# Performance work log

Measured on AMD Instinct MI355X. Metric: run time of the kernel, lower is better.

The kernel has to match this reference:

```python
import jax, jax.numpy as jnp
import numpy as np

B, S, D, H = 2, 2048, 1024, 16
HD = D // H  # head depth


def setup_inputs() -> dict:
    key = jax.random.key(0)
    ks = jax.random.split(key, 8)
    scale = 0.02
    K = jax.random.normal(ks[0], (B, S, D), jnp.float32)
    V = jax.random.normal(ks[1], (B, S, D), jnp.float32)
    Q = jax.random.normal(ks[2], (B, S, D), jnp.float32)
    # causal additive mask: 1.0 where attention is disallowed (strict upper triangle)
    mask = jnp.broadcast_to(
        jnp.triu(jnp.ones((S, S), jnp.float32), k=1)[None, None, :, :], (B, 1, S, S)
    )
    Wk = jax.random.normal(ks[3], (D, D), jnp.float32) * scale
    Wv = jax.random.normal(ks[4], (D, D), jnp.float32) * scale
    Wq = jax.random.normal(ks[5], (D, D), jnp.float32) * scale
    Wo = jax.random.normal(ks[6], (D, D), jnp.float32) * scale
    z = jnp.zeros((D,), jnp.float32)
    return {"K": K, "V": V, "Q": Q, "mask": mask,
            "Wk": Wk, "bk": z, "Wv": Wv, "bv": z,
            "Wq": Wq, "bq": z, "Wo": Wo, "bo": z}


def _split_heads(x):  # [B,S,D] -> [B,H,S,HD]
    return x.reshape(B, S, H, HD).transpose(0, 2, 1, 3)


def reference(K, V, Q, mask, Wk, bk, Wv, bv, Wq, bq, Wo, bo):
    k = _split_heads(K @ Wk + bk)
    v = _split_heads(V @ Wv + bv)
    q = _split_heads(Q @ Wq + bq)
    # NOTE: source scales by sqrt(d_model), not sqrt(head_depth)
    logits = jnp.einsum("bhqd,bhkd->bhqk", q, k) / jnp.sqrt(jnp.float32(D))
    logits = logits + mask * (-1e9)
    attn = jax.nn.softmax(logits, axis=-1)
    out = jnp.einsum("bhqk,bhkd->bhqd", attn, v)  # [B,H,S,HD]
    out = out.transpose(0, 2, 1, 3).reshape(B, S, D)
    return out @ Wo + bo
```

## Files before the change

kernel.cpp:

```cpp
#include <hip/hip_runtime.h>
#include <hip/hip_bf16.h>

typedef unsigned short u16;
typedef unsigned int u32;
typedef unsigned long long u64;
typedef __attribute__((ext_vector_type(8))) __bf16 bf16x8;
typedef __attribute__((ext_vector_type(4))) float f32x4;

#define SEQ 2048
#define DM 1024
#define NH 16
#define HDim 64

__device__ __forceinline__ float bf_lo(u32 u) { return __uint_as_float(u << 16); }
__device__ __forceinline__ float bf_hi(u32 u) { return __uint_as_float(u & 0xffff0000u); }
__device__ __forceinline__ u16 f2bf(float f) {
    u32 u = __float_as_uint(f);
    u32 r = (u + 0x7fffu + ((u >> 16) & 1u)) >> 16;
    return (u16)r;
}
__device__ __forceinline__ float bf2f(u16 h) { return __uint_as_float(((u32)h) << 16); }

__device__ __forceinline__ float fexp2(float x) {
#if __has_builtin(__builtin_amdgcn_exp2f)
    return __builtin_amdgcn_exp2f(x);
#else
    return __expf(x * 0.69314718056f);
#endif
}

#define GLD16(g, l)                                                         \
    __builtin_amdgcn_global_load_lds(                                       \
        (const __attribute__((address_space(1))) void*)(g),                 \
        (__attribute__((address_space(3))) void*)(l), 16, 0, 0)

#define VWAIT_BAR(N)                                                        \
    asm volatile("s_waitcnt vmcnt(" #N ")\n\ts_barrier" ::: "memory")
#define BAR_ONLY()  asm volatile("s_barrier" ::: "memory")

__device__ __forceinline__ bool detect_f32(const u32* q)
{
    const u32 w = q[threadIdx.x & 63];
    const int e0 = ((w & 0xffffu) >> 7) & 0xff;
    const int e1 = (w >> 23) & 0xff;
    const unsigned long long b = __ballot(e0 >= 0x90 || e1 >= 0x90);
    return b != 0ull;
}

__global__ __launch_bounds__(256)
void prep_all(const void* __restrict__ Qin, const void* __restrict__ Kin,
              const void* __restrict__ Vin,
              const void* __restrict__ w0, const void* __restrict__ w1,
              const void* __restrict__ w2, const void* __restrict__ w3,
              const void* __restrict__ b0, const void* __restrict__ b1,
              const void* __restrict__ b2, const void* __restrict__ b3,
              u16* __restrict__ Xall, u16* __restrict__ Wtall,
              u16* __restrict__ ball)
{
    __shared__ u16 T[64 * 66];
    const bool f = detect_f32((const u32*)Qin);
    const int t = threadIdx.x;
    const int bid = blockIdx.x;

    if (bid < 6144) {
        const int z = bid >> 11;
        const int bx = bid & 2047;
        const void* src = (z == 0) ? Qin : (z == 1) ? Kin : Vin;
        const size_t i0 = ((size_t)bx * 256 + t) * 8;
        u16* d = Xall + (size_t)z * 4194304 + i0;
        if (f) {
            const uint4* s = reinterpret_cast<const uint4*>((const float*)src + i0);
            uint4 a = s[0], b = s[1];
            u16 o[8];
            o[0] = f2bf(__uint_as_float(a.x)); o[1] = f2bf(__uint_as_float(a.y));
            o[2] = f2bf(__uint_as_float(a.z)); o[3] = f2bf(__uint_as_float(a.w));
            o[4] = f2bf(__uint_as_float(b.x)); o[5] = f2bf(__uint_as_float(b.y));
            o[6] = f2bf(__uint_as_float(b.z)); o[7] = f2bf(__uint_as_float(b.w));
            *reinterpret_cast<uint4*>(d) = *reinterpret_cast<const uint4*>(o);
        } else {
            *reinterpret_cast<uint4*>(d) =
                *reinterpret_cast<const uint4*>((const u16*)src + i0);
        }
    } else if (bid < 7168) {
        const int r = bid - 6144;
        const int z = r >> 8;
        const void* src = (z == 0) ? w0 : (z == 1) ? w1 : (z == 2) ? w2 : w3;
        const int n0 = ((r >> 4) & 15) * 64;
        const int k0 = (r & 15) * 64;
        const int c = t & 63, g = t >> 6;
        if (f) {
            const float* W = (const float*)src;
#pragma unroll
            for (int i = 0; i < 16; i++) {
                const int kl = g * 16 + i;
                T[kl * 66 + c] = f2bf(W[(size_t)(k0 + kl) * DM + n0 + c]);
            }
        } else {
            const u16* W = (const u16*)src;
#pragma unroll
            for (int i = 0; i < 16; i++) {
                const int kl = g * 16 + i;
                T[kl * 66 + c] = W[(size_t)(k0 + kl) * DM + n0 + c];
            }
        }
        __syncthreads();
        u16* dst = Wtall + (size_t)z * 1048576;
#pragma unroll
        for (int i = 0; i < 16; i++) {
            const int nl = g * 16 + i;
            dst[(size_t)(n0 + nl) * DM + k0 + c] = T[c * 66 + nl];
        }
    } else {
#pragma unroll
        for (int j = 0; j < 16; j++) {
            const int idx = t * 16 + j;
            const int z = idx >> 10, e = idx & 1023;
            const void* src = (z == 0) ? b0 : (z == 1) ? b1 : (z == 2) ? b2 : b3;
            ball[idx] = f ? f2bf(((const float*)src)[e]) : ((const u16*)src)[e];
        }
    }
}

__global__ __launch_bounds__(256)
void gemm128(const u16* __restrict__ Xall, const u16* __restrict__ Wtall,
             const u16* __restrict__ ball, u16* __restrict__ Yall)
{
    __shared__ __align__(16) u16 As[2][128 * 32];
    __shared__ __align__(16) u16 Bs[2][128 * 32];

    const int zz = blockIdx.z;
    const bool swp = (zz != 2);
    const u16* X  = Xall + (size_t)zz * 4194304;
    const u16* Wt = Wtall + (size_t)zz * 1048576;

    const int t    = threadIdx.x;
    const int w    = t >> 6;
    const int lane = t & 63;
    const int quad = lane >> 4;
    const int ln   = lane & 15;
    const int m0   = blockIdx.x * 128;
    const int n0   = blockIdx.y * 128;

    f32x4 acc[4][4];
#pragma unroll
    for (int i = 0; i < 4; i++)
#pragma unroll
        for (int j = 0; j < 4; j++) acc[i][j] = (f32x4){0.f, 0.f, 0.f, 0.f};

    const int swz = (lane >> 3) & 3;
    const u16* ag = X  + (size_t)(m0 + w * 32 + (lane >> 2)) * DM + ((lane & 3) ^ swz) * 8;
    const u16* bg = Wt + (size_t)(n0 + w * 32 + (lane >> 2)) * DM + ((lane & 3) ^ swz) * 8;

    const int wr = (w >> 1) * 64;
    const int wc = (w & 1) * 64;
    const int rs = (quad ^ ((ln >> 1) & 3)) * 8;

#define GSTAGE(B)                                        \
    {                                                    \
        GLD16(ag,           &As[B][w * 1024]);           \
        GLD16(ag + 16 * DM, &As[B][w * 1024 + 512]);     \
        GLD16(bg,           &Bs[B][w * 1024]);           \
        GLD16(bg + 16 * DM, &Bs[B][w * 1024 + 512]);     \
        ag += 32; bg += 32;                              \
    }

#define GCOMP(B)                                                              \
    {                                                                         \
        bf16x8 af[4], bfr[4];                                                 \
        _Pragma("unroll") for (int rt = 0; rt < 4; rt++)                      \
            af[rt] = *reinterpret_cast<const bf16x8*>(                        \
                &As[B][(wr + rt * 16 + ln) * 32 + rs]);                       \
        _Pragma("unroll") for (int ct = 0; ct < 4; ct++)                      \
            bfr[ct] = *reinterpret_cast<const bf16x8*>(                       \
                &Bs[B][(wc + ct * 16 + ln) * 32 + rs]);                       \
        if (swp) {                                                            \
            _Pragma("unroll") for (int rt = 0; rt < 4; rt++)                  \
                _Pragma("unroll") for (int ct = 0; ct < 4; ct++)              \
                    acc[rt][ct] = __builtin_amdgcn_mfma_f32_16x16x32_bf16(    \
                        bfr[ct], af[rt], acc[rt][ct], 0, 0, 0);               \
        } else {                                                              \
            _Pragma("unroll") for (int rt = 0; rt < 4; rt++)                  \
                _Pragma("unroll") for (int ct = 0; ct < 4; ct++)              \
                    acc[rt][ct] = __builtin_amdgcn_mfma_f32_16x16x32_bf16(    \
                        af[rt], bfr[ct], acc[rt][ct], 0, 0, 0);               \
        }                                                                     \
    }

    GSTAGE(0);
#pragma unroll 1
    for (int it = 0; it < 15; ++it) {
        GSTAGE(1);
        VWAIT_BAR(4);
        GCOMP(0);
        BAR_ONLY();
        GSTAGE(0);
        VWAIT_BAR(4);
        GCOMP(1);
        BAR_ONLY();
    }
    GSTAGE(1);
    VWAIT_BAR(4);
    GCOMP(0);
    BAR_ONLY();
    asm volatile("s_waitcnt vmcnt(0)" ::: "memory");
    __builtin_amdgcn_s_barrier();
    GCOMP(1);
#undef GSTAGE
#undef GCOMP

    u16* Y = Yall + (size_t)zz * 4194304;

    if (swp) {
        const float scale = (zz == 0) ? 0.04508422f : 1.0f;
#pragma unroll
        for (int ct = 0; ct < 4; ct++) {
            const int nb = n0 + wc + ct * 16 + quad * 4;
            const int h = nb >> 6, hd = nb & (HDim - 1);
            float bv[4];
#pragma unroll
            for (int r = 0; r < 4; r++) bv[r] = bf2f(ball[zz * 1024 + nb + r]);
#pragma unroll
            for (int rt = 0; rt < 4; rt++) {
                const int m = m0 + wr + rt * 16 + ln;
                const int b = m >> 11, s = m & (SEQ - 1);
                u16 o4[4];
#pragma unroll
                for (int r = 0; r < 4; r++)
                    o4[r] = f2bf((acc[rt][ct][r] + bv[r]) * scale);
                *reinterpret_cast<u64*>(
                    Y + (((size_t)(b * NH + h)) * SEQ + s) * HDim + hd) =
                    *reinterpret_cast<const u64*>(o4);
            }
        }
    } else {
#pragma unroll
        for (int ct = 0; ct < 4; ct++) {
            const int n = n0 + wc + ct * 16 + ln;
            const float bv = bf2f(ball[zz * 1024 + n]);
            const int h = n >> 6, hd = n & (HDim - 1);
#pragma unroll
            for (int rt = 0; rt < 4; rt++) {
                const int m = m0 + wr + rt * 16 + quad * 4;
                const int b = m >> 11, s = m & (SEQ - 1);
                u16 o4[4];
#pragma unroll
                for (int r = 0; r < 4; r++) o4[r] = f2bf(acc[rt][ct][r] + bv);
                *reinterpret_cast<u64*>(
                    Y + (((size_t)(b * NH + h) * HDim + hd) * SEQ + s)) =
                    *reinterpret_cast<const u64*>(o4);
            }
        }
    }
}

__device__ __forceinline__ void attn_tile2(
    const u16* __restrict__ Ks, const u16* __restrict__ Vs,
    u16* __restrict__ Ps, const bf16x8& qf0, const bf16x8& qf1,
    int kt, int qrow, int w, int quad, int ln, f32x4* o, float& l,
    bool diag)
{
    f32x4 s[4];
    __builtin_amdgcn_s_setprio(1);
#pragma unroll
    for (int ct = 0; ct < 4; ct++) {
        const u16* kr = &Ks[(ct * 16 + ln) * 72 + quad * 8];
        bf16x8 kf0 = *reinterpret_cast<const bf16x8*>(kr);
        bf16x8 kf1 = *reinterpret_cast<const bf16x8*>(kr + 32);
        f32x4 z = (f32x4){0.f, 0.f, 0.f, 0.f};
        z = __builtin_amdgcn_mfma_f32_16x16x32_bf16(kf0, qf0, z, 0, 0, 0);
        s[ct] = __builtin_amdgcn_mfma_f32_16x16x32_bf16(kf1, qf1, z, 0, 0, 0);
    }
    __builtin_amdgcn_s_setprio(0);
    const int kb = kt * 64 + quad * 4;
    float lacc = 0.f;
#pragma unroll
    for (int ct = 0; ct < 4; ct++) {
        float e0 = fexp2(s[ct][0]);
        float e1 = fexp2(s[ct][1]);
        float e2 = fexp2(s[ct][2]);
        float e3 = fexp2(s[ct][3]);
        if (diag) {
            const int kc = kb + ct * 16;
            e0 = (kc + 0 <= qrow) ? e0 : 0.f;
            e1 = (kc + 1 <= qrow) ? e1 : 0.f;
            e2 = (kc + 2 <= qrow) ? e2 : 0.f;
            e3 = (kc + 3 <= qrow) ? e3 : 0.f;
        }
        lacc += (e0 + e1) + (e2 + e3);
        u32 pk[2];
        asm("v_cvt_pk_bf16_f32 %0, %1, %2" : "=v"(pk[0]) : "v"(e0), "v"(e1));
        asm("v_cvt_pk_bf16_f32 %0, %1, %2" : "=v"(pk[1]) : "v"(e2), "v"(e3));
        *reinterpret_cast<u64*>(&Ps[(w * 16 + ln) * 72 + ct * 16 + quad * 4]) =
            *reinterpret_cast<const u64*>(pk);
    }
    l += lacc;
    __builtin_amdgcn_s_setprio(1);
#pragma unroll
    for (int ks = 0; ks < 2; ks++) {
        bf16x8 pf = *reinterpret_cast<const bf16x8*>(
            &Ps[(w * 16 + ln) * 72 + ks * 32 + quad * 8]);
#pragma unroll
        for (int nt = 0; nt < 4; nt++) {
            bf16x8 vf = *reinterpret_cast<const bf16x8*>(
                &Vs[(nt * 16 + ln) * 72 + ks * 32 + quad * 8]);
            o[nt] = __builtin_amdgcn_mfma_f32_16x16x32_bf16(pf, vf, o[nt], 0, 0, 0);
        }
    }
    __builtin_amdgcn_s_setprio(0);
}

__global__ __launch_bounds__(256)
void attn_split(const u16* __restrict__ qh, const u16* __restrict__ kh,
                const u16* __restrict__ vt, u16* __restrict__ Opart,
                float* __restrict__ Lpart)
{
    __shared__ __align__(16) u16 Ks[64 * 72];
    __shared__ __align__(16) u16 Vs[64 * 72];
    __shared__ __align__(16) u16 Ps[64 * 72];

    const int t    = threadIdx.x;
    const int L    = blockIdx.x + 16 * (blockIdx.y + 32 * blockIdx.z);
    const int xcd  = L & 7;
    const int slot = L >> 3;
    const int bh   = xcd + 8 * (slot >> 5);
    const int rr   = slot & 31;
    const int i    = rr & 15;
    const int c    = rr >> 4;

    const int w    = t >> 6;
    const int lane = t & 63;
    const int quad = lane >> 4;
    const int ln   = lane & 15;
    const int qtH  = 31 - i;
    const int qtL  = i;
    const int m    = (i >= 8) ? 8 : 16 - i;
    const int kt0  = c ? m : 0;
    const int kt1  = c ? (qtH + 1) : m;

    const size_t kbase = (size_t)bh * SEQ * HDim;
    const size_t vbase = (size_t)bh * HDim * SEQ;

    const u16* qrH = qh + kbase + (size_t)(qtH * 64 + w * 16 + ln) * HDim;
    const bf16x8 qfH0 = *reinterpret_cast<const bf16x8*>(qrH + quad * 8);
    const bf16x8 qfH1 = *reinterpret_cast<const bf16x8*>(qrH + 32 + quad * 8);
    const u16* qrL = qh + kbase + (size_t)(qtL * 64 + w * 16 + ln) * HDim;
    const bf16x8 qfL0 = *reinterpret_cast<const bf16x8*>(qrL + quad * 8);
    const bf16x8 qfL1 = *reinterpret_cast<const bf16x8*>(qrL + 32 + quad * 8);

    f32x4 oH[4], oL[4];
    float lH = 0.f, lL = 0.f;
#pragma unroll
    for (int k = 0; k < 4; k++) {
        oH[k] = (f32x4){0.f, 0.f, 0.f, 0.f};
        oL[k] = (f32x4){0.f, 0.f, 0.f, 0.f};
    }

    const int srow = t >> 2;
    const int sc   = (t & 3) * 16;
    const int rowH = qtH * 64 + w * 16 + ln;
    const int rowL = qtL * 64 + w * 16 + ln;

    uint4 kr0, kr1, vr0, vr1;
    {
        const uint4* ksp = reinterpret_cast<const uint4*>(
            kh + kbase + (size_t)(kt0 * 64 + srow) * HDim + sc);
        kr0 = ksp[0]; kr1 = ksp[1];
        const uint4* vsp = reinterpret_cast<const uint4*>(
            vt + vbase + (size_t)srow * SEQ + kt0 * 64 + sc);
        vr0 = vsp[0]; vr1 = vsp[1];
    }

    for (int kt = kt0; kt < kt1; kt++) {
        {
            uint4* kd = reinterpret_cast<uint4*>(&Ks[srow * 72 + sc]);
            kd[0] = kr0; kd[1] = kr1;
            uint4* vd = reinterpret_cast<uint4*>(&Vs[srow * 72 + sc]);
            vd[0] = vr0; vd[1] = vr1;
        }
        __syncthreads();

        if (kt + 1 < kt1) {
            const uint4* ksp = reinterpret_cast<const uint4*>(
                kh + kbase + (size_t)((kt + 1) * 64 + srow) * HDim + sc);
            kr0 = ksp[0]; kr1 = ksp[1];
            const uint4* vsp = reinterpret_cast<const uint4*>(
                vt + vbase + (size_t)srow * SEQ + (kt + 1) * 64 + sc);
            vr0 = vsp[0]; vr1 = vsp[1];
            __builtin_amdgcn_sched_barrier(0);
        }

        attn_tile2(Ks, Vs, Ps, qfH0, qfH1, kt, rowH, w, quad, ln, oH, lH,
                   kt == qtH);
        if (kt <= qtL)
            attn_tile2(Ks, Vs, Ps, qfL0, qfL1, kt, rowL, w, quad, ln, oL, lL,
                       kt == qtL);

        __syncthreads();
    }

    lH += __shfl_xor(lH, 16); lH += __shfl_xor(lH, 32);
    lL += __shfl_xor(lL, 16); lL += __shfl_xor(lL, 32);

    const size_t cb = ((size_t)c * 32 + bh) * SEQ;
    if (lane < 16) {
        Lpart[cb + qtH * 64 + w * 16 + lane] = lH;
        Lpart[cb + qtL * 64 + w * 16 + lane] = lL;
    }
#pragma unroll
    for (int r = 0; r < 4; r++) {
        const int rH = qtH * 64 + w * 16 + quad * 4 + r;
        const int rL = qtL * 64 + w * 16 + quad * 4 + r;
        u16* dH = Opart + (cb + rH) * HDim + ln;
        u16* dL = Opart + (cb + rL) * HDim + ln;
#pragma unroll
        for (int nt = 0; nt < 4; nt++) {
            dH[nt * 16] = f2bf(oH[nt][r]);
            dL[nt * 16] = f2bf(oL[nt][r]);
        }
    }
}

__global__ __launch_bounds__(256)
void attn_merge(const u16* __restrict__ Opart, const float* __restrict__ Lpart,
                u16* __restrict__ ctx)
{
    const size_t tid8 = (size_t)blockIdx.x * 256 + threadIdx.x;
    const int d8 = (int)(tid8 & 7);
    const int s  = (int)((tid8 >> 3) & (SEQ - 1));
    const int bh = (int)(tid8 >> 14);
    const size_t CSTR = (size_t)32 * SEQ * HDim;

    const uint4 a = *reinterpret_cast<const uint4*>(Opart + tid8 * 8);
    const uint4 b = *reinterpret_cast<const uint4*>(Opart + CSTR + tid8 * 8);
    const float l0 = Lpart[(size_t)bh * SEQ + s];
    const float l1 = Lpart[(size_t)32 * SEQ + (size_t)bh * SEQ + s];
    const float inv = 1.f / (l0 + l1);

    const u32 aw[4] = {a.x, a.y, a.z, a.w};
    const u32 bw[4] = {b.x, b.y, b.z, b.w};
    u32 ow[4];
#pragma unroll
    for (int p = 0; p < 4; p++) {
        const float lo = (bf_lo(aw[p]) + bf_lo(bw[p])) * inv;
        const float hi = (bf_hi(aw[p]) + bf_hi(bw[p])) * inv;
        ow[p] = (u32)f2bf(lo) | ((u32)f2bf(hi) << 16);
    }
    const int bb = bh >> 4, h = bh & 15;
    *reinterpret_cast<uint4*>(
        ctx + ((size_t)(bb * SEQ + s)) * DM + h * HDim + d8 * 8) =
        *reinterpret_cast<const uint4*>(ow);
}

__global__ __launch_bounds__(256)
void gemm_out(const u16* __restrict__ ctx, const u16* __restrict__ Wt,
              const u16* __restrict__ bias, void* __restrict__ dout,
              const u32* __restrict__ qdet)
{
    __shared__ __align__(16) u16 As[2][128 * 32];
    __shared__ __align__(16) u16 Bs[2][64 * 32];

    const int t    = threadIdx.x;
    const int w    = t >> 6;
    const int lane = t & 63;
    const int quad = lane >> 4;
    const int ln   = lane & 15;
    const int m0   = blockIdx.x * 128;
    const int n0   = blockIdx.y * 64;

    f32x4 acc[4][2];
#pragma unroll
    for (int i = 0; i < 4; i++)
#pragma unroll
        for (int j = 0; j < 2; j++) acc[i][j] = (f32x4){0.f, 0.f, 0.f, 0.f};

    const int swz = (lane >> 3) & 3;
    const u16* ag = ctx + (size_t)(m0 + w * 32 + (lane >> 2)) * DM + ((lane & 3) ^ swz) * 8;
    const u16* bg = Wt + (size_t)(n0 + w * 16 + (lane >> 2)) * DM + ((lane & 3) ^ swz) * 8;

    const int wr = (w >> 1) * 64;
    const int wc = (w & 1) * 32;
    const int rs = (quad ^ ((ln >> 1) & 3)) * 8;

#define OSTAGE(B)                                        \
    {                                                    \
        GLD16(ag,           &As[B][w * 1024]);           \
        GLD16(ag + 16 * DM, &As[B][w * 1024 + 512]);     \
        GLD16(bg,           &Bs[B][w * 512]);            \
        ag += 32; bg += 32;                              \
    }

#define OCOMP(B)                                                              \
    {                                                                         \
        bf16x8 af[4], bfr[2];                                                 \
        _Pragma("unroll") for (int rt = 0; rt < 4; rt++)                      \
            af[rt] = *reinterpret_cast<const bf16x8*>(                        \
                &As[B][(wr + rt * 16 + ln) * 32 + rs]);                       \
        _Pragma("unroll") for (int ct = 0; ct < 2; ct++)                      \
            bfr[ct] = *reinterpret_cast<const bf16x8*>(                       \
                &Bs[B][(wc + ct * 16 + ln) * 32 + rs]);                       \
        _Pragma("unroll") for (int rt = 0; rt < 4; rt++)                      \
            _Pragma("unroll") for (int ct = 0; ct < 2; ct++)                  \
                acc[rt][ct] = __builtin_amdgcn_mfma_f32_16x16x32_bf16(        \
                    af[rt], bfr[ct], acc[rt][ct], 0, 0, 0);                   \
    }

    OSTAGE(0);
#pragma unroll 1
    for (int it = 0; it < 15; ++it) {
        OSTAGE(1);
        VWAIT_BAR(3);
        OCOMP(0);
        BAR_ONLY();
        OSTAGE(0);
        VWAIT_BAR(3);
        OCOMP(1);
        BAR_ONLY();
    }
    OSTAGE(1);
    VWAIT_BAR(3);
    OCOMP(0);
    BAR_ONLY();
    asm volatile("s_waitcnt vmcnt(0)" ::: "memory");
    __builtin_amdgcn_s_barrier();
    OCOMP(1);
#undef OSTAGE
#undef OCOMP

    const bool f = detect_f32(qdet);
#pragma unroll
    for (int ct = 0; ct < 2; ct++) {
        const int n = n0 + wc + ct * 16 + ln;
        const float bv = bf2f(bias[n]);
#pragma unroll
        for (int rt = 0; rt < 4; rt++) {
            const int mb = m0 + wr + rt * 16 + quad * 4;
#pragma unroll
            for (int r = 0; r < 4; r++) {
                const float val = acc[rt][ct][r] + bv;
                if (f) ((float*)dout)[(size_t)(mb + r) * DM + n] = val;
                else   ((u16*)dout)[(size_t)(mb + r) * DM + n] = f2bf(val);
            }
        }
    }
}

__global__ __launch_bounds__(64)
void detect_dtype(const u32* __restrict__ q, int* __restrict__ flag)
{
    const int t = threadIdx.x;
    const u32 w = q[t];
    const int e0 = ((w & 0xffffu) >> 7) & 0xff;
    const int e1 = (w >> 23) & 0xff;
    const unsigned long long b = __ballot(e0 >= 0x90 || e1 >= 0x90);
    if (t == 0) *flag = (b != 0ull) ? 1 : 0;
}

struct AttnAcc { f32x4 o[4]; float l[4]; };

__device__ __forceinline__ void attn_tile(
    const u16* __restrict__ Ks, const u16* __restrict__ Vs,
    u16* __restrict__ Ps, const bf16x8& qf0, const bf16x8& qf1,
    int kt, int rowb, int w, int quad, int ln, AttnAcc& a)
{
    f32x4 s[4];
#pragma unroll
    for (int ct = 0; ct < 4; ct++) {
        const u16* kr = &Ks[(ct * 16 + ln) * 72 + quad * 8];
        bf16x8 kf0 = *reinterpret_cast<const bf16x8*>(kr);
        bf16x8 kf1 = *reinterpret_cast<const bf16x8*>(kr + 32);
        f32x4 z = (f32x4){0.f, 0.f, 0.f, 0.f};
        z = __builtin_amdgcn_mfma_f32_16x16x32_bf16(qf0, kf0, z, 0, 0, 0);
        s[ct] = __builtin_amdgcn_mfma_f32_16x16x32_bf16(qf1, kf1, z, 0, 0, 0);
    }
#pragma unroll
    for (int ct = 0; ct < 4; ct++) {
        const int kcol = kt * 64 + ct * 16 + ln;
#pragma unroll
        for (int r = 0; r < 4; r++) {
            const float e = (kcol <= rowb + r) ? __expf(s[ct][r]) : 0.f;
            a.l[r] += e;
            Ps[(w * 16 + quad * 4 + r) * 68 + ct * 16 + ln] = f2bf(e);
        }
    }
#pragma unroll
    for (int ks = 0; ks < 2; ks++) {
        bf16x8 pf = *reinterpret_cast<const bf16x8*>(
            &Ps[(w * 16 + ln) * 68 + ks * 32 + quad * 8]);
#pragma unroll
        for (int nt = 0; nt < 4; nt++) {
            bf16x8 vf = *reinterpret_cast<const bf16x8*>(
                &Vs[(nt * 16 + ln) * 72 + ks * 32 + quad * 8]);
            a.o[nt] = __builtin_amdgcn_mfma_f32_16x16x32_bf16(pf, vf, a.o[nt], 0, 0, 0);
        }
    }
}

__global__ __launch_bounds__(256)
void attn_mfma(const u16* __restrict__ qh, const u16* __restrict__ kh,
               const u16* __restrict__ vt, u16* __restrict__ ctx)
{
    __shared__ __align__(16) u16 Ks[64 * 72];
    __shared__ __align__(16) u16 Vs[64 * 72];
    __shared__ __align__(16) u16 Ps[64 * 68];

    const int t    = threadIdx.x;
    const int i    = blockIdx.x;
    const int bh   = blockIdx.y;
    const int w    = t >> 6;
    const int lane = t & 63;
    const int quad = lane >> 4;
    const int ln   = lane & 15;
    const int qtH  = 31 - i;
    const int qtL  = i;

    const size_t kbase = (size_t)bh * SEQ * HDim;
    const size_t vbase = (size_t)bh * HDim * SEQ;

    const u16* qrH = qh + kbase + (size_t)(qtH * 64 + w * 16 + ln) * HDim;
    const bf16x8 qfH0 = *reinterpret_cast<const bf16x8*>(qrH + quad * 8);
    const bf16x8 qfH1 = *reinterpret_cast<const bf16x8*>(qrH + 32 + quad * 8);
    const u16* qrL = qh + kbase + (size_t)(qtL * 64 + w * 16 + ln) * HDim;
    const bf16x8 qfL0 = *reinterpret_cast<const bf16x8*>(qrL + quad * 8);
    const bf16x8 qfL1 = *reinterpret_cast<const bf16x8*>(qrL + 32 + quad * 8);

    AttnAcc aH, aL;
#pragma unroll
    for (int k = 0; k < 4; k++) {
        aH.o[k] = (f32x4){0.f, 0.f, 0.f, 0.f}; aH.l[k] = 0.f;
        aL.o[k] = (f32x4){0.f, 0.f, 0.f, 0.f}; aL.l[k] = 0.f;
    }

    const int srow = t >> 2;
    const int sc   = (t & 3) * 16;
    const int rowHb = qtH * 64 + w * 16 + quad * 4;
    const int rowLb = qtL * 64 + w * 16 + quad * 4;

    for (int kt = 0; kt <= qtH; kt++) {
        {
            const uint4* ks = reinterpret_cast<const uint4*>(
                kh + kbase + (size_t)(kt * 64 + srow) * HDim + sc);
            uint4* kd = reinterpret_cast<uint4*>(&Ks[srow * 72 + sc]);
            kd[0] = ks[0];
            kd[1] = ks[1];
            const uint4* vs = reinterpret_cast<const uint4*>(
                vt + vbase + (size_t)srow * SEQ + kt * 64 + sc);
            uint4* vd = reinterpret_cast<uint4*>(&Vs[srow * 72 + sc]);
            vd[0] = vs[0];
            vd[1] = vs[1];
        }
        __syncthreads();

        attn_tile(Ks, Vs, Ps, qfH0, qfH1, kt, rowHb, w, quad, ln, aH);
        if (kt <= qtL)
            attn_tile(Ks, Vs, Ps, qfL0, qfL1, kt, rowLb, w, quad, ln, aL);

        __syncthreads();
    }

#pragma unroll
    for (int m = 1; m < 16; m <<= 1) {
#pragma unroll
        for (int r = 0; r < 4; r++) {
            aH.l[r] += __shfl_xor(aH.l[r], m);
            aL.l[r] += __shfl_xor(aL.l[r], m);
        }
    }

    const int b = bh >> 4;
    const int h = bh & 15;
#pragma unroll
    for (int r = 0; r < 4; r++) {
        const float invH = 1.f / aH.l[r];
        const float invL = 1.f / aL.l[r];
        const int sH = qtH * 64 + w * 16 + quad * 4 + r;
        const int sL = qtL * 64 + w * 16 + quad * 4 + r;
        u16* dH = ctx + ((size_t)(b * SEQ + sH)) * DM + h * HDim + ln;
        u16* dL = ctx + ((size_t)(b * SEQ + sL)) * DM + h * HDim + ln;
#pragma unroll
        for (int nt = 0; nt < 4; nt++) {
            dH[nt * 16] = f2bf(aH.o[nt][r] * invH);
            dL[nt * 16] = f2bf(aL.o[nt][r] * invL);
        }
    }
}

__global__ __launch_bounds__(256)
void gemm_bias(const void* __restrict__ Xv, const void* __restrict__ Wv,
               const void* __restrict__ biasv, void* __restrict__ Yv,
               int M, int N, int K, int mode, int xsel, int wsel, int ysel,
               float scale, const int* __restrict__ flagp)
{
    __shared__ __align__(16) u16 As[64 * 32];
    __shared__ __align__(16) u16 Bs[64 * 40];

    const int f  = *flagp;
    const bool xf = (xsel != 0) && (f != 0);
    const bool wf = (wsel != 0) && (f != 0);
    const bool yf = (ysel != 0) && (f != 0);

    const u16*   Xb = (const u16*)Xv;
    const float* Xf = (const float*)Xv;
    const u16*   Wb = (const u16*)Wv;
    const float* Wf = (const float*)Wv;

    const int t    = threadIdx.x;
    const int m0   = blockIdx.y * 64;
    const int n0   = blockIdx.x * 64;
    const int w    = t >> 6;
    const int lane = t & 63;
    const int quad = lane >> 4;
    const int ln   = lane & 15;

    f32x4 acc[4];
#pragma unroll
    for (int i = 0; i < 4; i++) acc[i] = (f32x4){0.f, 0.f, 0.f, 0.f};

    const int a_row = t >> 2;
    const int a_c8  = (t & 3) * 8;
    const int b_n   = t & 63;
    const int b_k8  = (t >> 6) * 8;

    for (int kk = 0; kk < K; kk += 32) {
        const size_t aoff = (size_t)(m0 + a_row) * K + kk + a_c8;
        if (!xf) {
            *reinterpret_cast<uint4*>(&As[a_row * 32 + a_c8]) =
                *reinterpret_cast<const uint4*>(Xb + aoff);
        } else {
            const float* src = Xf + aoff;
            uint4 u0 = reinterpret_cast<const uint4*>(src)[0];
            uint4 u1 = reinterpret_cast<const uint4*>(src)[1];
            u16 tmp[8];
            tmp[0] = f2bf(__uint_as_float(u0.x));
            tmp[1] = f2bf(__uint_as_float(u0.y));
            tmp[2] = f2bf(__uint_as_float(u0.z));
            tmp[3] = f2bf(__uint_as_float(u0.w));
            tmp[4] = f2bf(__uint_as_float(u1.x));
            tmp[5] = f2bf(__uint_as_float(u1.y));
            tmp[6] = f2bf(__uint_as_float(u1.z));
            tmp[7] = f2bf(__uint_as_float(u1.w));
            *reinterpret_cast<uint4*>(&As[a_row * 32 + a_c8]) =
                *reinterpret_cast<const uint4*>(tmp);
        }
        u16 tmp[8];
        if (!wf) {
#pragma unroll
            for (int j = 0; j < 8; j++)
                tmp[j] = Wb[(size_t)(kk + b_k8 + j) * N + n0 + b_n];
        } else {
#pragma unroll
            for (int j = 0; j < 8; j++)
                tmp[j] = f2bf(Wf[(size_t)(kk + b_k8 + j) * N + n0 + b_n]);
        }
        *reinterpret_cast<uint4*>(&Bs[b_n * 40 + b_k8]) =
            *reinterpret_cast<const uint4*>(tmp);

        __syncthreads();

        bf16x8 bfrag = *reinterpret_cast<const bf16x8*>(&Bs[(w * 16 + ln) * 40 + quad * 8]);
#pragma unroll
        for (int rt = 0; rt < 4; rt++) {
            bf16x8 afrag = *reinterpret_cast<const bf16x8*>(&As[(rt * 16 + ln) * 32 + quad * 8]);
            acc[rt] = __builtin_amdgcn_mfma_f32_16x16x32_bf16(afrag, bfrag, acc[rt], 0, 0, 0);
        }
        __syncthreads();
    }

    const int n = n0 + w * 16 + ln;
    const float bv = wf ? ((const float*)biasv)[n] : bf2f(((const u16*)biasv)[n]);
#pragma unroll
    for (int rt = 0; rt < 4; rt++) {
        if (mode == 2) {
            const int m = m0 + rt * 16 + quad * 4;
            const int b = m >> 11;
            const int s = m & (SEQ - 1);
            const int h = n >> 6;
            const int hd = n & (HDim - 1);
            u16 o4[4];
#pragma unroll
            for (int r = 0; r < 4; r++) o4[r] = f2bf((acc[rt][r] + bv) * scale);
            *reinterpret_cast<u64*>(
                (u16*)Yv + (((size_t)(b * NH + h) * HDim + hd) * SEQ + s)) =
                *reinterpret_cast<const u64*>(o4);
        } else {
#pragma unroll
            for (int r = 0; r < 4; r++) {
                const int m = m0 + rt * 16 + quad * 4 + r;
                const float val = (acc[rt][r] + bv) * scale;
                if (mode == 0) {
                    if (yf) ((float*)Yv)[(size_t)m * N + n] = val;
                    else    ((u16*)Yv)[(size_t)m * N + n] = f2bf(val);
                } else {
                    const int b = m >> 11;
                    const int s = m & (SEQ - 1);
                    const int h = n >> 6;
                    const int hd = n & (HDim - 1);
                    ((u16*)Yv)[(((size_t)(b * NH + h)) * SEQ + s) * HDim + hd] = f2bf(val);
                }
            }
        }
    }
}

extern "C" void kernel_launch(void* const* d_in, const int* in_sizes, int n_in,
                              void* d_out, int out_size, void* d_ws, size_t ws_size,
                              hipStream_t stream)
{
    const void* Kin = d_in[0];
    const void* Vin = d_in[1];
    const void* Qin = d_in[2];
    const void* Wk = d_in[4];
    const void* bk = d_in[5];
    const void* Wv = d_in[6];
    const void* bv = d_in[7];
    const void* Wq = d_in[8];
    const void* bq = d_in[9];
    const void* Wo = d_in[10];
    const void* bo = d_in[11];

    char* ws = (char*)d_ws;
    const size_t NEED = ((size_t)29360128 + 4096) * 2 + 256;

    if (ws_size >= NEED) {
        u16* Xall  = (u16*)ws;
        u16* Yall  = (u16*)ws + 12582912;
        u16* Wtall = (u16*)ws + 25165824;
        u16* ball  = (u16*)ws + 29360128;
        u16* qhp   = Yall;
        u16* khp   = Yall + 4194304;
        u16* vtp   = Yall + 8388608;
        u16* ctx   = Xall;
        u16* Opart = Xall + 4194304;
        float* Lpart = (float*)Wtall;

        hipLaunchKernelGGL(prep_all, dim3(7169), dim3(256), 0, stream,
                           Qin, Kin, Vin, Wq, Wk, Wv, Wo, bq, bk, bv, bo,
                           Xall, Wtall, ball);

        hipLaunchKernelGGL(gemm128, dim3(32, 8, 3), dim3(256), 0, stream,
                           Xall, Wtall, ball, Yall);

        hipLaunchKernelGGL(attn_split, dim3(16, 32, 2), dim3(256), 0, stream,
                           qhp, khp, vtp, Opart, Lpart);

        hipLaunchKernelGGL(attn_merge, dim3(2048), dim3(256), 0, stream,
                           Opart, Lpart, ctx);

        hipLaunchKernelGGL(gemm_out, dim3(32, 16), dim3(256), 0, stream,
                           ctx, Wtall + (size_t)3 * 1048576, ball + 3 * 1024,
                           d_out, (const u32*)Qin);
    } else {
        const size_t SEG = (size_t)2 * SEQ * DM * sizeof(u16);
        u16* qh  = (u16*)(ws);
        u16* khd = (u16*)(ws + SEG);
        u16* vtd = (u16*)(ws + 2 * SEG);
        u16* ctx = (u16*)(ws + 3 * SEG);
        int* flag = (int*)(ws + 4 * SEG);

        hipLaunchKernelGGL(detect_dtype, dim3(1), dim3(64), 0, stream,
                           (const u32*)Qin, flag);

        const int M = 2 * SEQ;
        dim3 ggrid(DM / 64, M / 64);
        dim3 gblk(256);

        hipLaunchKernelGGL(gemm_bias, ggrid, gblk, 0, stream, Qin, Wq, bq, qh,  M, DM, DM, 1, 1, 1, 0, 0.03125f, flag);
        hipLaunchKernelGGL(gemm_bias, ggrid, gblk, 0, stream, Kin, Wk, bk, khd, M, DM, DM, 1, 1, 1, 0, 1.0f,     flag);
        hipLaunchKernelGGL(gemm_bias, ggrid, gblk, 0, stream, Vin, Wv, bv, vtd, M, DM, DM, 2, 1, 1, 0, 1.0f,     flag);

        hipLaunchKernelGGL(attn_mfma, dim3(16, 2 * NH), dim3(256), 0,
                           stream, qh, khd, vtd, ctx);

        hipLaunchKernelGGL(gemm_bias, ggrid, gblk, 0, stream, ctx, Wo, bo, d_out, M, DM, DM, 0, 0, 1, 1, 1.0f, flag);
    }
}
```

Baseline: 254.1 us.

## Fuse attention split-merge into output projection GEMM A-tile load

Removes the separate attn_merge kernel. The output projection GEMM now loads both partial attention outputs and their softmax denominators directly, merges and normalizes them in registers, and writes the bf16 A tile into LDS itself. This saves one launch and a full write and read of the context tensor. In exchange, the A operand goes through registers instead of async global-to-LDS loads, each block redoes the merge for every N tile (16 times), and the QKV GEMM and output GEMM switch their hand-placed waitcnt/barrier pipelining to plain __syncthreads.

Result: no change. 259.0 us (+1.9%).

```diff
diff --git a/kernel.cpp b/kernel.cpp
--- a/kernel.cpp
+++ b/kernel.cpp
@@ -29,14 +29,26 @@
 #endif
 }
 
+__device__ __forceinline__ float frcp(float x) {
+#if __has_builtin(__builtin_amdgcn_rcpf)
+    return __builtin_amdgcn_rcpf(x);
+#else
+    return 1.0f / x;
+#endif
+}
+
+__device__ __forceinline__ u32 merge2(u32 a, u32 b, float inv) {
+    const float lo = (bf_lo(a) + bf_lo(b)) * inv;
+    const float hi = (bf_hi(a) + bf_hi(b)) * inv;
+    u32 r;
+    asm("v_cvt_pk_bf16_f32 %0, %1, %2" : "=v"(r) : "v"(lo), "v"(hi));
+    return r;
+}
+
 #define GLD16(g, l)                                                         \
     __builtin_amdgcn_global_load_lds(                                       \
         (const __attribute__((address_space(1))) void*)(g),                 \
         (__attribute__((address_space(3))) void*)(l), 16, 0, 0)
-
-#define VWAIT_BAR(N)                                                        \
-    asm volatile("s_waitcnt vmcnt(" #N ")\n\ts_barrier" ::: "memory")
-#define BAR_ONLY()  asm volatile("s_barrier" ::: "memory")
 
 __device__ __forceinline__ bool detect_f32(const u32* q)
 {
@@ -187,23 +199,13 @@
     }
 
     GSTAGE(0);
+    __syncthreads();
 #pragma unroll 1
     for (int it = 0; it < 15; ++it) {
-        GSTAGE(1);
-        VWAIT_BAR(4);
-        GCOMP(0);
-        BAR_ONLY();
-        GSTAGE(0);
-        VWAIT_BAR(4);
-        GCOMP(1);
-        BAR_ONLY();
-    }
-    GSTAGE(1);
-    VWAIT_BAR(4);
-    GCOMP(0);
-    BAR_ONLY();
-    asm volatile("s_waitcnt vmcnt(0)" ::: "memory");
-    __builtin_amdgcn_s_barrier();
+        GSTAGE(1); GCOMP(0); __syncthreads();
+        GSTAGE(0); GCOMP(1); __syncthreads();
+    }
+    GSTAGE(1); GCOMP(0); __syncthreads();
     GCOMP(1);
 #undef GSTAGE
 #undef GCOMP
@@ -421,43 +423,14 @@
 }
 
 __global__ __launch_bounds__(256)
-void attn_merge(const u16* __restrict__ Opart, const float* __restrict__ Lpart,
-                u16* __restrict__ ctx)
-{
-    const size_t tid8 = (size_t)blockIdx.x * 256 + threadIdx.x;
-    const int d8 = (int)(tid8 & 7);
-    const int s  = (int)((tid8 >> 3) & (SEQ - 1));
-    const int bh = (int)(tid8 >> 14);
-    const size_t CSTR = (size_t)32 * SEQ * HDim;
-
-    const uint4 a = *reinterpret_cast<const uint4*>(Opart + tid8 * 8);
-    const uint4 b = *reinterpret_cast<const uint4*>(Opart + CSTR + tid8 * 8);
-    const float l0 = Lpart[(size_t)bh * SEQ + s];
-    const float l1 = Lpart[(size_t)32 * SEQ + (size_t)bh * SEQ + s];
-    const float inv = 1.f / (l0 + l1);
-
-    const u32 aw[4] = {a.x, a.y, a.z, a.w};
-    const u32 bw[4] = {b.x, b.y, b.z, b.w};
-    u32 ow[4];
-#pragma unroll
-    for (int p = 0; p < 4; p++) {
-        const float lo = (bf_lo(aw[p]) + bf_lo(bw[p])) * inv;
-        const float hi = (bf_hi(aw[p]) + bf_hi(bw[p])) * inv;
-        ow[p] = (u32)f2bf(lo) | ((u32)f2bf(hi) << 16);
-    }
-    const int bb = bh >> 4, h = bh & 15;
-    *reinterpret_cast<uint4*>(
-        ctx + ((size_t)(bb * SEQ + s)) * DM + h * HDim + d8 * 8) =
-        *reinterpret_cast<const uint4*>(ow);
-}
-
-__global__ __launch_bounds__(256)
-void gemm_out(const u16* __restrict__ ctx, const u16* __restrict__ Wt,
-              const u16* __restrict__ bias, void* __restrict__ dout,
-              const u32* __restrict__ qdet)
+void gemm_out(const u16* __restrict__ Opart, const float* __restrict__ Lpart,
+              const u16* __restrict__ Wt, const u16* __restrict__ bias,
+              void* __restrict__ dout, const u32* __restrict__ qdet)
 {
     __shared__ __align__(16) u16 As[2][128 * 32];
     __shared__ __align__(16) u16 Bs[2][64 * 32];
+
+    const size_t CSTR = (size_t)32 * SEQ * HDim;
 
     const int t    = threadIdx.x;
     const int w    = t >> 6;
@@ -474,19 +447,53 @@
         for (int j = 0; j < 2; j++) acc[i][j] = (f32x4){0.f, 0.f, 0.f, 0.f};
 
     const int swz = (lane >> 3) & 3;
-    const u16* ag = ctx + (size_t)(m0 + w * 32 + (lane >> 2)) * DM + ((lane & 3) ^ swz) * 8;
-    const u16* bg = Wt + (size_t)(n0 + w * 16 + (lane >> 2)) * DM + ((lane & 3) ^ swz) * 8;
+    const int g8  = ((lane & 3) ^ swz) * 8;
+    const int r1  = m0 + w * 32 + (lane >> 2);
+    const int b16 = (r1 >> 11) * 16;
+    const int s1  = r1 & (SEQ - 1);
+    const u16* bg = Wt + (size_t)(n0 + w * 16 + (lane >> 2)) * DM + g8;
 
     const int wr = (w >> 1) * 64;
     const int wc = (w & 1) * 32;
     const int rs = (quad ^ ((ln >> 1) & 3)) * 8;
 
-#define OSTAGE(B)                                        \
+    uint4 pa0, pa1, pb0, pb1;
+    float inv1, inv2;
+
+#define OALOAD(kk)                                                            \
+    {                                                                         \
+        const int col = (kk) + g8;                                            \
+        const int bh  = b16 + (col >> 6);                                     \
+        const int hd  = col & 63;                                             \
+        const size_t e1 = ((size_t)bh * SEQ + s1) * HDim + hd;                \
+        const size_t e2 = e1 + 16 * HDim;                                     \
+        pa0 = *reinterpret_cast<const uint4*>(Opart + e1);                    \
+        pa1 = *reinterpret_cast<const uint4*>(Opart + CSTR + e1);             \
+        pb0 = *reinterpret_cast<const uint4*>(Opart + e2);                    \
+        pb1 = *reinterpret_cast<const uint4*>(Opart + CSTR + e2);             \
+        inv1 = frcp(Lpart[(size_t)bh * SEQ + s1] +                            \
+                    Lpart[(size_t)(32 + bh) * SEQ + s1]);                     \
+        inv2 = frcp(Lpart[(size_t)bh * SEQ + s1 + 16] +                       \
+                    Lpart[(size_t)(32 + bh) * SEQ + s1 + 16]);                \
+    }
+
+#define OAWRITE(B)                                                            \
+    {                                                                         \
+        u32 o[4];                                                             \
+        o[0] = merge2(pa0.x, pa1.x, inv1); o[1] = merge2(pa0.y, pa1.y, inv1); \
+        o[2] = merge2(pa0.z, pa1.z, inv1); o[3] = merge2(pa0.w, pa1.w, inv1); \
+        *reinterpret_cast<uint4*>(&As[B][w * 1024 + lane * 8]) =              \
+            *reinterpret_cast<const uint4*>(o);                               \
+        o[0] = merge2(pb0.x, pb1.x, inv2); o[1] = merge2(pb0.y, pb1.y, inv2); \
+        o[2] = merge2(pb0.z, pb1.z, inv2); o[3] = merge2(pb0.w, pb1.w, inv2); \
+        *reinterpret_cast<uint4*>(&As[B][w * 1024 + 512 + lane * 8]) =        \
+            *reinterpret_cast<const uint4*>(o);                               \
+    }
+
+#define OBSTAGE(B)                                       \
     {                                                    \
-        GLD16(ag,           &As[B][w * 1024]);           \
-        GLD16(ag + 16 * DM, &As[B][w * 1024 + 512]);     \
-        GLD16(bg,           &Bs[B][w * 512]);            \
-        ag += 32; bg += 32;                              \
+        GLD16(bg, &Bs[B][w * 512]);                      \
+        bg += 32;                                        \
     }
 
 #define OCOMP(B)                                                              \
@@ -504,26 +511,24 @@
                     af[rt], bfr[ct], acc[rt][ct], 0, 0, 0);                   \
     }
 
-    OSTAGE(0);
+    OALOAD(0); OBSTAGE(0); OAWRITE(0);
+    __syncthreads();
+    int kk = 32;
 #pragma unroll 1
     for (int it = 0; it < 15; ++it) {
-        OSTAGE(1);
-        VWAIT_BAR(3);
-        OCOMP(0);
-        BAR_ONLY();
-        OSTAGE(0);
-        VWAIT_BAR(3);
-        OCOMP(1);
-        BAR_ONLY();
-    }
-    OSTAGE(1);
-    VWAIT_BAR(3);
-    OCOMP(0);
-    BAR_ONLY();
-    asm volatile("s_waitcnt vmcnt(0)" ::: "memory");
-    __builtin_amdgcn_s_barrier();
+        OALOAD(kk); OBSTAGE(1); OCOMP(0); OAWRITE(1);
+        __syncthreads();
+        kk += 32;
+        OALOAD(kk); OBSTAGE(0); OCOMP(1); OAWRITE(0);
+        __syncthreads();
+        kk += 32;
+    }
+    OALOAD(kk); OBSTAGE(1); OCOMP(0); OAWRITE(1);
+    __syncthreads();
     OCOMP(1);
-#undef OSTAGE
+#undef OALOAD
+#undef OAWRITE
+#undef OBSTAGE
 #undef OCOMP
 
     const bool f = detect_f32(qdet);
@@ -828,7 +833,6 @@
         u16* qhp   = Yall;
         u16* khp   = Yall + 4194304;
         u16* vtp   = Yall + 8388608;
-        u16* ctx   = Xall;
         u16* Opart = Xall + 4194304;
         float* Lpart = (float*)Wtall;
 
@@ -842,12 +846,9 @@
         hipLaunchKernelGGL(attn_split, dim3(16, 32, 2), dim3(256), 0, stream,
                            qhp, khp, vtp, Opart, Lpart);
 
-        hipLaunchKernelGGL(attn_merge, dim3(2048), dim3(256), 0, stream,
-                           Opart, Lpart, ctx);
-
         hipLaunchKernelGGL(gemm_out, dim3(32, 16), dim3(256), 0, stream,
-                           ctx, Wtall + (size_t)3 * 1048576, ball + 3 * 1024,
-                           d_out, (const u32*)Qin);
+                           Opart, Lpart, Wtall + (size_t)3 * 1048576,
+                           ball + 3 * 1024, d_out, (const u32*)Qin);
     } else {
         const size_t SEG = (size_t)2 * SEQ * DM * sizeof(u16);
         u16* qh  = (u16*)(ws);
```
